# Optimization experiments

Hardware: AMD Instinct MI355X
Metric: run time of the kernel (lower is better)

## Reference

```python
import jax, jax.numpy as jnp
import numpy as np

B, H, N_CHAR, MAX_LEN = 512, 1024, 128, 256


def setup_inputs() -> dict:
    key = jax.random.key(0)
    ks = jax.random.split(key, 8)
    s = 1.0 / np.sqrt(H)  # PyTorch LSTMCell/Linear uniform init scale
    hid = jax.random.normal(ks[0], (B, H), dtype=jnp.float32)
    cell0 = jax.random.normal(ks[1], (B, H), dtype=jnp.float32)
    # constant start-token one-hot input (input0_tensor in the original)
    inp0 = jnp.zeros((B, N_CHAR), dtype=jnp.float32).at[:, 0].set(1.0)
    W_ih = jax.random.uniform(ks[2], (4 * H, N_CHAR + H), jnp.float32, -s, s)
    W_hh = jax.random.uniform(ks[3], (4 * H, H), jnp.float32, -s, s)
    b_ih = jax.random.uniform(ks[4], (4 * H,), jnp.float32, -s, s)
    b_hh = jax.random.uniform(ks[5], (4 * H,), jnp.float32, -s, s)
    W_out = jax.random.uniform(ks[6], (N_CHAR, H), jnp.float32, -s, s)
    b_out = jax.random.uniform(ks[7], (N_CHAR,), jnp.float32, -s, s)
    return {"hid": hid, "inp0": inp0, "cell0": cell0,
            "W_ih": W_ih, "W_hh": W_hh, "b_ih": b_ih, "b_hh": b_hh,
            "W_out": W_out, "b_out": b_out}


def reference(hid, inp0, cell0, W_ih, W_hh, b_ih, b_hh, W_out, b_out):
    # x_t = concat(inp0, h) is constant in its first N_CHAR columns, so
    # precompute inp0's contribution once (same math as cat + single GEMM).
    x_part = inp0 @ W_ih[:, :N_CHAR].T + b_ih + b_hh  # (B, 4H)
    W_ih_h = W_ih[:, N_CHAR:]  # (4H, H) acting on h

    def step(carry, _):
        h, c = carry
        gates = x_part + h @ W_ih_h.T + h @ W_hh.T  # (B, 4H)
        i, f, g, o = jnp.split(gates, 4, axis=1)  # PyTorch gate order i,f,g,o
        c = jax.nn.sigmoid(f) * c + jax.nn.sigmoid(i) * jnp.tanh(g)
        h = jax.nn.sigmoid(o) * jnp.tanh(c)
        return (h, c), h @ W_out.T + b_out  # logits (B, N_CHAR)

    _, outs = jax.lax.scan(step, (hid, cell0), None, length=MAX_LEN)
    # outs: (max_len, B, N_CHAR) -> (B, N_CHAR, max_len) to match torch.stack(dim=2)
    return jnp.transpose(outs, (1, 2, 0))
```

## Files before the change

### kernel.cpp

```cpp
#include <hip/hip_runtime.h>
#include <hip/hip_bf16.h>


using bf16 = __hip_bfloat16;
typedef short bf16x8 __attribute__((ext_vector_type(8)));
typedef float f32x4  __attribute__((ext_vector_type(4)));
typedef float f32x16 __attribute__((ext_vector_type(16)));

static constexpr int BATCH = 512;
static constexpr int HID   = 1024;
static constexpr int NCH   = 128;
static constexpr int TLEN  = 256;
static constexpr int NP    = 4096;

static constexpr size_t OFF_WP  = 0;
static constexpr size_t OFF_WOB = OFF_WP  + (size_t)NP * HID * 2;
static constexpr size_t OFF_HB0 = OFF_WOB + (size_t)NCH * HID * 2;
static constexpr size_t OFF_HB1 = OFF_HB0 + (size_t)BATCH * HID * 2;
static constexpr size_t OFF_XP  = OFF_HB1 + (size_t)BATCH * HID * 2;
static constexpr size_t OFF_BAR = OFF_XP  + (size_t)BATCH * NP * 4;

__device__ __forceinline__ float sigm(float x) { return 1.f / (1.f + __expf(-x)); }

__device__ __forceinline__ unsigned short f2bf(float x) {
  unsigned u = __float_as_uint(x);
  return (unsigned short)((u + 0x7FFFu + ((u >> 16) & 1u)) >> 16);
}

__device__ __forceinline__ int rowp_to_n(int rp) {
  int jg = rp >> 6, c = rp & 63;
  return (c >> 4) * HID + jg * 16 + (c & 15);
}

__global__ void prep_misc(const float* __restrict__ hid0, const float* __restrict__ wout,
                          bf16* __restrict__ hb0, bf16* __restrict__ wob,
                          unsigned* __restrict__ bar)
{
  int gid = blockIdx.x * blockDim.x + threadIdx.x;
  int stride = gridDim.x * blockDim.x;
  for (int i = gid; i < BATCH * HID; i += stride) hb0[i] = __float2bfloat16(hid0[i]);
  for (int i = gid; i < NCH * HID;  i += stride) wob[i] = __float2bfloat16(wout[i]);
  if (gid < 1024) bar[gid] = 0u;
}

__global__ void prep_wp(const float* __restrict__ W_ih, const float* __restrict__ W_hh,
                        bf16* __restrict__ wp)
{
  int gid = blockIdx.x * blockDim.x + threadIdx.x;
  int stride = gridDim.x * blockDim.x;
  for (int i = gid; i < NP * HID; i += stride) {
    int rp = i >> 10, k = i & 1023;
    int n = rowp_to_n(rp);
    float v = W_ih[(size_t)n * 1152 + 128 + k] + W_hh[(size_t)n * 1024 + k];
    wp[i] = __float2bfloat16(v);
  }
}

__global__ void prep_xp(const float* __restrict__ inp0, const float* __restrict__ W_ih,
                        const float* __restrict__ b_ih, const float* __restrict__ b_hh,
                        float* __restrict__ xp)
{
  int b = blockIdx.x;
  const float4* ip = (const float4*)(inp0 + b * NCH);
  for (int rp = threadIdx.x; rp < NP; rp += blockDim.x) {
    int n = rowp_to_n(rp);
    const float4* wr = (const float4*)(W_ih + (size_t)n * 1152);
    float acc = b_ih[n] + b_hh[n];
    #pragma unroll 8
    for (int q = 0; q < 32; ++q) {
      float4 a = ip[q], w = wr[q];
      acc += a.x * w.x + a.y * w.y + a.z * w.z + a.w * w.w;
    }
    xp[(size_t)b * NP + rp] = acc;
  }
}

__launch_bounds__(256, 1)
__global__ void lstm_main(const bf16* __restrict__ wp, const bf16* __restrict__ wob,
                          const float* __restrict__ xp, const float* __restrict__ cell0,
                          const float* __restrict__ bout,
                          bf16* __restrict__ hb0, bf16* __restrict__ hb1,
                          float* __restrict__ out, unsigned* __restrict__ bar)
{
  __shared__ bf16 wlds[64 * HID];
  __shared__ float obuf[16][16][17];
  __shared__ float opart[4][16][16];
  __shared__ int s_pop[8];

  const int tid  = threadIdx.x;
  const int bx   = blockIdx.x;
  const int lane = tid & 63;
  const int wv   = tid >> 6;
  const int bm   = bx >> 6;
  const int jg   = bx & 63;
  const int wrow = bm * 128 + wv * 32;
  const int l31  = lane & 31;
  const int lhi  = lane >> 5;
  const bool low = (l31 < 16);
  const int jj   = lane & 15;
  const int jcol = jg * 16 + jj;

  {
    const char* src = (const char*)(wp + (size_t)jg * 64 * HID);
    for (int it = tid; it < 8192; it += 256) {
      int r  = it >> 7;
      int kb = (it & 127) << 4;
      bf16x8 v = *(const bf16x8*)(src + r * 2048 + kb);
      *(bf16x8*)((char*)wlds + r * 2048 + (kb ^ ((r & 15) << 4))) = v;
    }
  }

  f32x16 xpA, xpB;
  #pragma unroll
  for (int q = 0; q < 16; ++q) {
    int rr = (q & 3) + ((q >> 2) << 3) + (lhi << 2);
    const float* xr = xp + (size_t)(wrow + rr) * NP + jg * 64;
    xpA[q] = xr[l31];
    xpB[q] = xr[32 + l31];
  }

  float creg[8];
  #pragma unroll
  for (int q = 0; q < 8; ++q) {
    int rr = (q & 3) + ((q >> 2) << 3) + (lhi << 2) + (low ? 0 : 16);
    creg[q] = cell0[(size_t)(wrow + rr) * HID + jcol];
  }

  const int omt = (bx >> 3) << 4;
  const int ont = (bx & 7) << 4;
  const float bo = bout[ont + jj];

  const int myx = __builtin_amdgcn_s_getreg(6164) & 7;
  if (tid == 0) {
    __hip_atomic_fetch_add(bar + (size_t)myx * 32, 1u, __ATOMIC_RELAXED, __HIP_MEMORY_SCOPE_AGENT);
    __threadfence();
    __hip_atomic_fetch_add(bar + (size_t)8 * 32, 1u, __ATOMIC_RELEASE, __HIP_MEMORY_SCOPE_AGENT);
    int it = 0;
    while (__hip_atomic_load(bar + (size_t)8 * 32, __ATOMIC_RELAXED, __HIP_MEMORY_SCOPE_AGENT) < 256u) {
      __builtin_amdgcn_s_sleep(1);
      if ((++it & 255) == 0) __builtin_amdgcn_fence(__ATOMIC_ACQUIRE, "agent");
    }
  }
  __syncthreads();
  if (tid < 8)
    s_pop[tid] = (int)__hip_atomic_load(bar + (size_t)tid * 32, __ATOMIC_RELAXED, __HIP_MEMORY_SCOPE_AGENT);
  __syncthreads();
  int nx = 0, tot = 0;
  #pragma unroll
  for (int i = 0; i < 8; ++i) { nx += (s_pop[i] != 0) ? 1 : 0; tot += s_pop[i]; }
  const bool elect = (nx >= 2) && (tot == 256);
  const unsigned mypop = (unsigned)s_pop[myx];
  const unsigned NF = elect ? (unsigned)nx : 256u;
  unsigned* const xcdCnt = bar + (size_t)(16 + myx) * 32;
  unsigned* const gCnt   = bar + (size_t)24 * 32;
  unsigned* const epochX = bar + (size_t)(800 + myx * 16);

  __syncthreads();

  for (int t = 0; t <= TLEN; ++t) {
    const bf16* __restrict__ hcur = (t & 1) ? hb1 : hb0;
    bf16* __restrict__ hnxt = (t & 1) ? hb0 : hb1;

    if (t >= 1) {
      f32x4 oacc = {0.f, 0.f, 0.f, 0.f};
      const int kq = (lane >> 4) << 3;
      const bf16* ap = hcur + (size_t)(omt + jj) * HID + kq;
      const bf16* bp = wob + (size_t)(ont + jj) * HID + kq;
      #pragma unroll
      for (int ks = wv * 8; ks < wv * 8 + 8; ++ks) {
        bf16x8 av = *(const bf16x8*)(ap + ks * 32);
        bf16x8 bv = *(const bf16x8*)(bp + ks * 32);
        oacc = __builtin_amdgcn_mfma_f32_16x16x32_bf16(av, bv, oacc, 0, 0, 0);
      }
      #pragma unroll
      for (int q = 0; q < 4; ++q)
        opart[wv][((lane >> 4) << 2) + q][jj] = oacc[q];
    }
    __syncthreads();
    if (t >= 1) {
      const int orow = tid >> 4, ocol = tid & 15;
      float s = opart[0][orow][ocol] + opart[1][orow][ocol]
              + opart[2][orow][ocol] + opart[3][orow][ocol];
      obuf[orow][ocol][(t - 1) & 15] = s + bo;
    }

    if ((t & 15) == 0 && t >= 16) {
      __syncthreads();
      const int orow = tid >> 4, ocol = tid & 15;
      float* dst = out + ((size_t)(omt + orow) * NCH + (ont + ocol)) * TLEN + (t - 16);
      #pragma unroll
      for (int s = 0; s < 16; ++s) dst[s] = obuf[orow][ocol][s];
    }

    if (t == TLEN) break;

    f32x16 accA = xpA, accB = xpB;
    {
      const bf16* ap = hcur + (size_t)(wrow + l31) * HID + (lhi << 3);
      const char* wb = (const char*)wlds;
      const int base0 = l31 * 2048;
      const int sxor  = (l31 & 15) << 4;
      const int kb4   = lhi << 4;
      #pragma unroll 16
      for (int ks = 0; ks < 64; ++ks) {
        bf16x8 av = *(const bf16x8*)(ap + ks * 16);
        const int ko = ((ks << 5) | kb4) ^ sxor;
        bf16x8 b0 = *(const bf16x8*)(wb + base0 + ko);
        bf16x8 b1 = *(const bf16x8*)(wb + base0 + 65536 + ko);
        accA = __builtin_amdgcn_mfma_f32_32x32x16_bf16(av, b0, accA, 0, 0, 0);
        accB = __builtin_amdgcn_mfma_f32_32x32x16_bf16(av, b1, accB, 0, 0, 0);
      }
    }

    float s0[16], s1[16], u0[16], u1[16];
    #pragma unroll
    for (int q = 0; q < 16; ++q) {
      s0[q] = sigm(accA[q]);
      float a1 = accB[q];
      float sg = sigm(low ? 2.f * a1 : a1);
      s1[q] = low ? 2.f * sg - 1.f : sg;
    }
    #pragma unroll
    for (int q = 0; q < 16; ++q) {
      u0[q] = __shfl_xor(s0[q], 16);
      u1[q] = __shfl_xor(s1[q], 16);
    }

    {
      unsigned* const h32 = (unsigned*)hnxt;
      #pragma unroll
      for (int q = 0; q < 8; ++q) {
        float fg  = low ? u0[q]         : s0[q + 8];
        float ig  = low ? s0[q] * s1[q] : u0[q + 8] * u1[q + 8];
        float og  = low ? u1[q]         : s1[q + 8];
        float cn  = fg * creg[q] + ig;
        creg[q] = cn;
        float hv = og * (2.f * sigm(2.f * cn) - 1.f);
        unsigned v = (unsigned)f2bf(hv);
        unsigned p = (unsigned)__shfl_xor((int)v, 1);
        if (!(lane & 1)) {
          int rr = (q & 3) + ((q >> 2) << 3) + (lhi << 2) + (low ? 0 : 16);
          __hip_atomic_store(&h32[((size_t)(wrow + rr) << 9) + (jcol >> 1)],
                             v | (p << 16), __ATOMIC_RELAXED, __HIP_MEMORY_SCOPE_AGENT);
        }
      }
    }

    asm volatile("s_waitcnt vmcnt(0)" ::: "memory");
    __syncthreads();
    if (tid == 0) {
      unsigned old = __hip_atomic_fetch_add(xcdCnt, 1u, __ATOMIC_RELAXED, __HIP_MEMORY_SCOPE_AGENT);
      const bool lastx = !elect || (old == mypop * (unsigned)(t + 1) - 1u);
      if (lastx) {
        if (elect) {
          __hip_atomic_fetch_add(gCnt, 1u, __ATOMIC_RELAXED, __HIP_MEMORY_SCOPE_AGENT);
        } else {
          __threadfence();
          __hip_atomic_fetch_add(gCnt, 1u, __ATOMIC_RELEASE, __HIP_MEMORY_SCOPE_AGENT);
        }
      }
      if (!elect) {
        const unsigned tgt = NF * (unsigned)(t + 1);
        int it = 0;
        while (__hip_atomic_load(gCnt, __ATOMIC_RELAXED, __HIP_MEMORY_SCOPE_AGENT) < tgt) {
          __builtin_amdgcn_s_sleep(1);
          if ((++it & 255) == 0) __builtin_amdgcn_fence(__ATOMIC_ACQUIRE, "agent");
        }
      } else if (lastx) {
        const unsigned tgt = (unsigned)nx * (unsigned)(t + 1);
        int it = 0;
        while (__hip_atomic_load(gCnt, __ATOMIC_RELAXED, __HIP_MEMORY_SCOPE_AGENT) < tgt) {
          __builtin_amdgcn_s_sleep(1);
          if ((++it & 255) == 0) __builtin_amdgcn_fence(__ATOMIC_ACQUIRE, "agent");
        }
        __builtin_amdgcn_fence(__ATOMIC_ACQUIRE, "agent");
        __hip_atomic_store(epochX, (unsigned)(t + 1), __ATOMIC_RELAXED, __HIP_MEMORY_SCOPE_AGENT);
      } else {
        const unsigned want = (unsigned)(t + 1);
        int it = 0; bool ok = false;
        while (true) {
          if (__hip_atomic_load(epochX, __ATOMIC_RELAXED, __HIP_MEMORY_SCOPE_AGENT) >= want) { ok = true; break; }
          __builtin_amdgcn_s_sleep(1);
          if (++it > (1 << 18)) break;
        }
        if (ok) {
          asm volatile("buffer_inv" ::: "memory");
        } else {
          const unsigned tgt = (unsigned)nx * (unsigned)(t + 1);
          int it2 = 0;
          while (__hip_atomic_load(gCnt, __ATOMIC_RELAXED, __HIP_MEMORY_SCOPE_AGENT) < tgt) {
            __builtin_amdgcn_s_sleep(1);
            if ((++it2 & 255) == 0) __builtin_amdgcn_fence(__ATOMIC_ACQUIRE, "agent");
          }
          __threadfence();
        }
      }
    }
    if (!elect) {
      if (tid < 64) __builtin_amdgcn_fence(__ATOMIC_ACQUIRE, "agent");
    }
    __syncthreads();
  }
}

extern "C" void kernel_launch(void* const* d_in, const int* in_sizes, int n_in,
                              void* d_out, int out_size, void* d_ws, size_t ws_size,
                              hipStream_t stream)
{
  const float* hid0  = (const float*)d_in[0];
  const float* inp0  = (const float*)d_in[1];
  const float* cell0 = (const float*)d_in[2];
  const float* W_ih  = (const float*)d_in[3];
  const float* W_hh  = (const float*)d_in[4];
  const float* b_ih  = (const float*)d_in[5];
  const float* b_hh  = (const float*)d_in[6];
  const float* W_out = (const float*)d_in[7];
  const float* b_out = (const float*)d_in[8];
  float* out = (float*)d_out;

  char* ws = (char*)d_ws;
  bf16* wp      = (bf16*)(ws + OFF_WP);
  bf16* wob     = (bf16*)(ws + OFF_WOB);
  bf16* hb0     = (bf16*)(ws + OFF_HB0);
  bf16* hb1     = (bf16*)(ws + OFF_HB1);
  float* xp     = (float*)(ws + OFF_XP);
  unsigned* bar = (unsigned*)(ws + OFF_BAR);

  prep_misc<<<512, 256, 0, stream>>>(hid0, W_out, hb0, wob, bar);
  prep_wp<<<4096, 256, 0, stream>>>(W_ih, W_hh, wp);
  prep_xp<<<512, 256, 0, stream>>>(inp0, W_ih, b_ih, b_hh, xp);

  void* args[] = { &wp, &wob, &xp, &cell0, &b_out, &hb0, &hb1, &out, &bar };
  hipError_t e = hipLaunchCooperativeKernel(lstm_main, dim3(256), dim3(256), args, 0u, stream);
  if (e != hipSuccess) {
    lstm_main<<<dim3(256), dim3(256), 0, stream>>>(wp, wob, xp, cell0, b_out,
                                                   hb0, hb1, out, bar);
  }
}
```

Measured before the change: 3.765 ms.

## Overlap output projection with the grid barrier wait

Reorders each timestep so the output logits GEMM runs after the block signals arrival at the grid barrier but before it waits. Waves 1-3 compute the projection, split over about 11 k-steps each, while wave 0 (tid 0) spins on the barrier. The aim is to hide the projection latency inside the barrier wait. In exchange the loop gains an extra iteration and a later flush of the output buffer, and the projection work on waves 1-3 is heavier.

```diff
diff --git a/kernel.cpp b/kernel.cpp
--- a/kernel.cpp
+++ b/kernel.cpp
@@ -84,7 +84,7 @@
 {
   __shared__ bf16 wlds[64 * HID];
   __shared__ float obuf[16][16][17];
-  __shared__ float opart[4][16][16];
+  __shared__ float opart[3][16][16];
   __shared__ int s_pop[8];
 
   const int tid  = threadIdx.x;
@@ -157,108 +157,106 @@
 
   __syncthreads();
 
-  for (int t = 0; t <= TLEN; ++t) {
+  for (int t = 0; t <= TLEN + 1; ++t) {
     const bf16* __restrict__ hcur = (t & 1) ? hb1 : hb0;
     bf16* __restrict__ hnxt = (t & 1) ? hb0 : hb1;
 
-    if (t >= 1) {
+    if (t >= 17 && ((t - 17) & 15) == 0) {
+      const int orow = tid >> 4, ocol = tid & 15;
+      float* dst = out + ((size_t)(omt + orow) * NCH + (ont + ocol)) * TLEN + (t - 17);
+      #pragma unroll
+      for (int s = 0; s < 16; ++s) dst[s] = obuf[orow][ocol][s];
+    }
+
+    bool lastx = false;
+    if (t < TLEN) {
+      f32x16 accA = xpA, accB = xpB;
+      {
+        const bf16* ap = hcur + (size_t)(wrow + l31) * HID + (lhi << 3);
+        const char* wb = (const char*)wlds;
+        const int base0 = l31 * 2048;
+        const int sxor  = (l31 & 15) << 4;
+        const int kb4   = lhi << 4;
+        #pragma unroll 16
+        for (int ks = 0; ks < 64; ++ks) {
+          bf16x8 av = *(const bf16x8*)(ap + ks * 16);
+          const int ko = ((ks << 5) | kb4) ^ sxor;
+          bf16x8 b0 = *(const bf16x8*)(wb + base0 + ko);
+          bf16x8 b1 = *(const bf16x8*)(wb + base0 + 65536 + ko);
+          accA = __builtin_amdgcn_mfma_f32_32x32x16_bf16(av, b0, accA, 0, 0, 0);
+          accB = __builtin_amdgcn_mfma_f32_32x32x16_bf16(av, b1, accB, 0, 0, 0);
+        }
+      }
+
+      float s0[16], s1[16], u0[16], u1[16];
+      #pragma unroll
+      for (int q = 0; q < 16; ++q) {
+        s0[q] = sigm(accA[q]);
+        float a1 = accB[q];
+        float sg = sigm(low ? 2.f * a1 : a1);
+        s1[q] = low ? 2.f * sg - 1.f : sg;
+      }
+      #pragma unroll
+      for (int q = 0; q < 16; ++q) {
+        u0[q] = __shfl_xor(s0[q], 16);
+        u1[q] = __shfl_xor(s1[q], 16);
+      }
+
+      {
+        unsigned* const h32 = (unsigned*)hnxt;
+        #pragma unroll
+        for (int q = 0; q < 8; ++q) {
+          float fg  = low ? u0[q]         : s0[q + 8];
+          float ig  = low ? s0[q] * s1[q] : u0[q + 8] * u1[q + 8];
+          float og  = low ? u1[q]         : s1[q + 8];
+          float cn  = fg * creg[q] + ig;
+          creg[q] = cn;
+          float hv = og * (2.f * sigm(2.f * cn) - 1.f);
+          unsigned v = (unsigned)f2bf(hv);
+          unsigned p = (unsigned)__shfl_xor((int)v, 1);
+          if (!(lane & 1)) {
+            int rr = (q & 3) + ((q >> 2) << 3) + (lhi << 2) + (low ? 0 : 16);
+            __hip_atomic_store(&h32[((size_t)(wrow + rr) << 9) + (jcol >> 1)],
+                               v | (p << 16), __ATOMIC_RELAXED, __HIP_MEMORY_SCOPE_AGENT);
+          }
+        }
+      }
+
+      asm volatile("s_waitcnt vmcnt(0)" ::: "memory");
+      __syncthreads();
+      if (tid == 0) {
+        unsigned old = __hip_atomic_fetch_add(xcdCnt, 1u, __ATOMIC_RELAXED, __HIP_MEMORY_SCOPE_AGENT);
+        lastx = !elect || (old == mypop * (unsigned)(t + 1) - 1u);
+        if (lastx) {
+          if (elect) {
+            __hip_atomic_fetch_add(gCnt, 1u, __ATOMIC_RELAXED, __HIP_MEMORY_SCOPE_AGENT);
+          } else {
+            __threadfence();
+            __hip_atomic_fetch_add(gCnt, 1u, __ATOMIC_RELEASE, __HIP_MEMORY_SCOPE_AGENT);
+          }
+        }
+      }
+    }
+
+    if (t >= 1 && t <= TLEN && wv > 0) {
       f32x4 oacc = {0.f, 0.f, 0.f, 0.f};
       const int kq = (lane >> 4) << 3;
-      const bf16* ap = hcur + (size_t)(omt + jj) * HID + kq;
-      const bf16* bp = wob + (size_t)(ont + jj) * HID + kq;
-      #pragma unroll
-      for (int ks = wv * 8; ks < wv * 8 + 8; ++ks) {
-        bf16x8 av = *(const bf16x8*)(ap + ks * 32);
-        bf16x8 bv = *(const bf16x8*)(bp + ks * 32);
-        oacc = __builtin_amdgcn_mfma_f32_16x16x32_bf16(av, bv, oacc, 0, 0, 0);
+      const bf16* ap2 = hcur + (size_t)(omt + jj) * HID + kq;
+      const bf16* bp2 = wob + (size_t)(ont + jj) * HID + kq;
+      const int k0 = (wv - 1) * 11;
+      const int k1 = (k0 + 11 < 32) ? k0 + 11 : 32;
+      #pragma unroll 4
+      for (int ks = k0; ks < k1; ++ks) {
+        bf16x8 avv = *(const bf16x8*)(ap2 + ks * 32);
+        bf16x8 bvv = *(const bf16x8*)(bp2 + ks * 32);
+        oacc = __builtin_amdgcn_mfma_f32_16x16x32_bf16(avv, bvv, oacc, 0, 0, 0);
       }
       #pragma unroll
       for (int q = 0; q < 4; ++q)
-        opart[wv][((lane >> 4) << 2) + q][jj] = oacc[q];
-    }
-    __syncthreads();
-    if (t >= 1) {
-      const int orow = tid >> 4, ocol = tid & 15;
-      float s = opart[0][orow][ocol] + opart[1][orow][ocol]
-              + opart[2][orow][ocol] + opart[3][orow][ocol];
-      obuf[orow][ocol][(t - 1) & 15] = s + bo;
-    }
-
-    if ((t & 15) == 0 && t >= 16) {
-      __syncthreads();
-      const int orow = tid >> 4, ocol = tid & 15;
-      float* dst = out + ((size_t)(omt + orow) * NCH + (ont + ocol)) * TLEN + (t - 16);
-      #pragma unroll
-      for (int s = 0; s < 16; ++s) dst[s] = obuf[orow][ocol][s];
-    }
-
-    if (t == TLEN) break;
-
-    f32x16 accA = xpA, accB = xpB;
-    {
-      const bf16* ap = hcur + (size_t)(wrow + l31) * HID + (lhi << 3);
-      const char* wb = (const char*)wlds;
-      const int base0 = l31 * 2048;
-      const int sxor  = (l31 & 15) << 4;
-      const int kb4   = lhi << 4;
-      #pragma unroll 16
-      for (int ks = 0; ks < 64; ++ks) {
-        bf16x8 av = *(const bf16x8*)(ap + ks * 16);
-        const int ko = ((ks << 5) | kb4) ^ sxor;
-        bf16x8 b0 = *(const bf16x8*)(wb + base0 + ko);
-        bf16x8 b1 = *(const bf16x8*)(wb + base0 + 65536 + ko);
-        accA = __builtin_amdgcn_mfma_f32_32x32x16_bf16(av, b0, accA, 0, 0, 0);
-        accB = __builtin_amdgcn_mfma_f32_32x32x16_bf16(av, b1, accB, 0, 0, 0);
-      }
-    }
-
-    float s0[16], s1[16], u0[16], u1[16];
-    #pragma unroll
-    for (int q = 0; q < 16; ++q) {
-      s0[q] = sigm(accA[q]);
-      float a1 = accB[q];
-      float sg = sigm(low ? 2.f * a1 : a1);
-      s1[q] = low ? 2.f * sg - 1.f : sg;
-    }
-    #pragma unroll
-    for (int q = 0; q < 16; ++q) {
-      u0[q] = __shfl_xor(s0[q], 16);
-      u1[q] = __shfl_xor(s1[q], 16);
-    }
-
-    {
-      unsigned* const h32 = (unsigned*)hnxt;
-      #pragma unroll
-      for (int q = 0; q < 8; ++q) {
-        float fg  = low ? u0[q]         : s0[q + 8];
-        float ig  = low ? s0[q] * s1[q] : u0[q + 8] * u1[q + 8];
-        float og  = low ? u1[q]         : s1[q + 8];
-        float cn  = fg * creg[q] + ig;
-        creg[q] = cn;
-        float hv = og * (2.f * sigm(2.f * cn) - 1.f);
-        unsigned v = (unsigned)f2bf(hv);
-        unsigned p = (unsigned)__shfl_xor((int)v, 1);
-        if (!(lane & 1)) {
-          int rr = (q & 3) + ((q >> 2) << 3) + (lhi << 2) + (low ? 0 : 16);
-          __hip_atomic_store(&h32[((size_t)(wrow + rr) << 9) + (jcol >> 1)],
-                             v | (p << 16), __ATOMIC_RELAXED, __HIP_MEMORY_SCOPE_AGENT);
-        }
-      }
-    }
-
-    asm volatile("s_waitcnt vmcnt(0)" ::: "memory");
-    __syncthreads();
-    if (tid == 0) {
-      unsigned old = __hip_atomic_fetch_add(xcdCnt, 1u, __ATOMIC_RELAXED, __HIP_MEMORY_SCOPE_AGENT);
-      const bool lastx = !elect || (old == mypop * (unsigned)(t + 1) - 1u);
-      if (lastx) {
-        if (elect) {
-          __hip_atomic_fetch_add(gCnt, 1u, __ATOMIC_RELAXED, __HIP_MEMORY_SCOPE_AGENT);
-        } else {
-          __threadfence();
-          __hip_atomic_fetch_add(gCnt, 1u, __ATOMIC_RELEASE, __HIP_MEMORY_SCOPE_AGENT);
-        }
-      }
+        opart[wv - 1][((lane >> 4) << 2) + q][jj] = oacc[q];
+    }
+
+    if (t < TLEN && tid == 0) {
       if (!elect) {
         const unsigned tgt = NF * (unsigned)(t + 1);
         int it = 0;
@@ -296,8 +294,13 @@
         }
       }
     }
-    if (!elect) {
-      if (tid < 64) __builtin_amdgcn_fence(__ATOMIC_ACQUIRE, "agent");
+    if (t < TLEN && !elect && tid < 64) __builtin_amdgcn_fence(__ATOMIC_ACQUIRE, "agent");
+    __syncthreads();
+
+    if (t >= 1 && t <= TLEN) {
+      const int orow = tid >> 4, ocol = tid & 15;
+      float s = opart[0][orow][ocol] + opart[1][orow][ocol] + opart[2][orow][ocol];
+      obuf[orow][ocol][(t - 1) & 15] = s + bo;
     }
     __syncthreads();
   }
```

Result: no change. 3.777 ms (+0.3%).
